# Optimization experiments

Hardware: AMD Instinct MI355X
Metric: run time of the kernel (lower is better)

Reference implementation:

```python
import jax, jax.numpy as jnp
import numpy as np

DIM = 1536; NH = 12; HD = 128; C2 = HD // 2          # rope half-dim = 64
F, H, W = 1, 30, 52
FRAME = H * W                                         # 1560 tokens/frame
SINK_FRAMES = 1; LOCAL_ATTN = 6
SINK = SINK_FRAMES * FRAME                            # 1560
MAX_ATTN = LOCAL_ATTN * 1560                          # 9360
CACHE = 9360                                          # kv cache length
GLOBAL_END = 9360; LOCAL_END_CACHE = 9360             # cache state before step
SPLITS = (C2 - 2 * (C2 // 3), C2 // 3, C2 // 3)       # (22, 21, 21)
EPS = 1e-6


def setup_inputs() -> dict:
    key = jax.random.key(0)
    ks = jax.random.split(key, 12)
    s = F * H * W
    rn = lambda k, sh, sc=1.0: jax.random.normal(k, sh, jnp.float32) * sc
    x = rn(ks[0], (1, s, DIM))
    Wq = rn(ks[1], (DIM, DIM), 0.02); Wk = rn(ks[2], (DIM, DIM), 0.02)
    Wv = rn(ks[3], (DIM, DIM), 0.02); Wo = rn(ks[4], (DIM, DIM), 0.02)
    zb = jnp.zeros((DIM,), jnp.float32)
    angles = jax.random.uniform(ks[5], (1024, C2), jnp.float32) * (2.0 * np.pi)
    freqs_cos = jnp.cos(angles); freqs_sin = jnp.sin(angles)
    cache_k = rn(ks[6], (1, CACHE, NH, HD)); cache_v = rn(ks[7], (1, CACHE, NH, HD))
    return dict(x=x, Wq=Wq, bq=zb, Wk=Wk, bk=zb, Wv=Wv, bv=zb, Wo=Wo, bo=zb,
                nq_w=jnp.ones((DIM,), jnp.float32), nk_w=jnp.ones((DIM,), jnp.float32),
                cache_k=cache_k, cache_v=cache_v,
                freqs_cos=freqs_cos, freqs_sin=freqs_sin,
                seq_lens=jnp.array([s], jnp.int32),
                grid_sizes=jnp.array([[F, H, W]], jnp.int32),
                current_start=GLOBAL_END)


def _rmsnorm(x, w):
    return x * jax.lax.rsqrt(jnp.mean(x * x, -1, keepdims=True) + EPS) * w


def _grid_table(table, start_frame):
    """table [1024, C2] -> per-token rope factors [S, 1, C2] over the (F,H,W) grid."""
    s0, s1, s2 = SPLITS
    tf, th, tw = table[:, :s0], table[:, s0:s0 + s1], table[:, s0 + s1:]
    fp = jnp.broadcast_to(tf[start_frame:start_frame + F][:, None, None, :], (F, H, W, s0))
    hp = jnp.broadcast_to(th[:H][None, :, None, :], (F, H, W, s1))
    wp = jnp.broadcast_to(tw[:W][None, None, :, :], (F, H, W, s2))
    return jnp.concatenate([fp, hp, wp], -1).reshape(F * H * W, 1, C2)


def _rope(x, cos, sin):
    # x: [b, s, n, d]; cos/sin: [s, 1, C2] (complex multiply in real arithmetic)
    b, s, n, d = x.shape
    xp = x.reshape(b, s, n, d // 2, 2)
    xr, xi = xp[..., 0], xp[..., 1]
    c, sn = cos[None], sin[None]                      # [1, s, 1, C2]
    out_r = xr * c - xi * sn
    out_i = xr * sn + xi * c
    return jnp.stack([out_r, out_i], -1).reshape(b, s, n, d)


def reference(x, Wq, bq, Wk, bk, Wv, bv, Wo, bo, nq_w, nk_w,
              cache_k, cache_v, freqs_cos, freqs_sin,
              seq_lens, grid_sizes, current_start):
    b, s = x.shape[:2]
    q = _rmsnorm(x @ Wq.T + bq, nq_w).reshape(b, s, NH, HD)
    k = _rmsnorm(x @ Wk.T + bk, nk_w).reshape(b, s, NH, HD)
    v = (x @ Wv.T + bv).reshape(b, s, NH, HD)

    start_frame = int(current_start) // FRAME
    cos = _grid_table(freqs_cos, start_frame)
    sin = _grid_table(freqs_sin, start_frame)
    rq = _rope(q, cos, sin)
    rk = _rope(k, cos, sin)

    # --- static cache bookkeeping (roll_and_insert path; all Python ints) ---
    num_new = s
    current_end = int(current_start) + num_new
    num_evicted = num_new + LOCAL_END_CACHE - CACHE           # 1560
    num_rolled = LOCAL_END_CACHE - num_evicted - SINK         # 6240
    local_end = LOCAL_END_CACHE + current_end - GLOBAL_END - num_evicted  # 9360
    local_start = local_end - num_new                         # 7800 == SINK + num_rolled
    temp_k = jnp.concatenate(
        [cache_k[:, :SINK], cache_k[:, SINK + num_evicted:SINK + num_evicted + num_rolled], rk], axis=1)
    temp_v = jnp.concatenate(
        [cache_v[:, :SINK], cache_v[:, SINK + num_evicted:SINK + num_evicted + num_rolled], v], axis=1)

    # --- sink + sliding-window attention ---
    local_budget = MAX_ATTN - SINK
    win_start = max(SINK, local_end - local_budget)
    k_cat = jnp.concatenate([temp_k[:, :SINK], temp_k[:, win_start:local_end]], axis=1)
    v_cat = jnp.concatenate([temp_v[:, :SINK], temp_v[:, win_start:local_end]], axis=1)

    logits = jnp.einsum('bqhd,bkhd->bhqk', rq, k_cat) * (HD ** -0.5)
    probs = jax.nn.softmax(logits, axis=-1)
    out = jnp.einsum('bhqk,bkhd->bqhd', probs, v_cat)
    y = out.reshape(b, s, DIM) @ Wo.T + bo
    return y
```

## Files before the change

### kernel.cpp

```cpp
#include <hip/hip_runtime.h>
#include <hip/hip_bf16.h>

typedef __bf16 bf16;
typedef __bf16 bf16x2 __attribute__((ext_vector_type(2)));
typedef __bf16 bf16x4 __attribute__((ext_vector_type(4)));
typedef __bf16 bf16x8 __attribute__((ext_vector_type(8)));
typedef float f32x4 __attribute__((ext_vector_type(4)));

#define DIM 1536
#define NH 12
#define HD 128
#define SEQ 1560
#define KV 9360
#define KVP 9408
#define SINK 1560
#define NEWBASE 7800
#define QSCALE 0.08838834764831845f
#define NSPLIT 3
#define CHUNK 3136
#define NT 49
#define QBLK 128
#define NQT 13

__device__ __forceinline__ void gl_lds16(const void* g, void* l) {
  __builtin_amdgcn_global_load_lds(
      (const __attribute__((address_space(1))) unsigned int*)g,
      (__attribute__((address_space(3))) unsigned int*)l, 16, 0, 0);
}

__global__ __launch_bounds__(256) void castk(const float* __restrict__ src,
                                             bf16* __restrict__ dst, int n) {
  int i = (blockIdx.x * 256 + threadIdx.x) * 8;
  if (i < n) {
    float4 a = *(const float4*)(src + i);
    float4 b = *(const float4*)(src + i + 4);
    bf16x8 o;
    o[0] = (bf16)a.x; o[1] = (bf16)a.y; o[2] = (bf16)a.z; o[3] = (bf16)a.w;
    o[4] = (bf16)b.x; o[5] = (bf16)b.y; o[6] = (bf16)b.z; o[7] = (bf16)b.w;
    *(bf16x8*)(dst + i) = o;
  }
}

struct GemmBatch {
  const bf16* B[3];
  const float* bias[3];
  float* C[3];
};

#define BM 128
#define BN 128
#define BK 32

__global__ __launch_bounds__(256, 2) void gemm_bt(const bf16* __restrict__ A,
                                                  GemmBatch gb, int M) {
  const bf16* Bw = gb.B[blockIdx.z];
  const float* bias = gb.bias[blockIdx.z];
  float* C = gb.C[blockIdx.z];
  int bm = blockIdx.x * BM;
  int bn = blockIdx.y * BN;

  __shared__ bf16 Alds[2][BM][BK];
  __shared__ bf16 Blds[2][BN][BK];

  int t = threadIdx.x;
  int lane = t & 63;
  int wave = t >> 6;
  int wr = wave >> 1, wc = wave & 1;
  int fr = lane & 15;
  int fo = (lane >> 4) * 8;

  f32x4 acc[4][4] = {};

  const int NK = DIM / BK;
  int colA = (lane & 3) * 8;
  int lrow = lane >> 2;

#define STAGEG(buf, k0)                                                     \
  {                                                                         \
    _Pragma("unroll") for (int p = 0; p < 2; ++p) {                         \
      int rbase = wave * 16 + p * 64;                                       \
      int ga = bm + rbase + lrow;                                           \
      if (ga > M - 1) ga = M - 1;                                           \
      gl_lds16(A + (size_t)ga * DIM + (k0) + colA, &Alds[buf][rbase][0]);   \
      int gbv = bn + rbase + lrow;                                          \
      gl_lds16(Bw + (size_t)gbv * DIM + (k0) + colA, &Blds[buf][rbase][0]); \
    }                                                                       \
  }

  STAGEG(0, 0);
  int cur = 0;
  for (int ks = 0; ks < NK; ++ks) {
    __syncthreads();
    if (ks + 1 < NK) STAGEG(cur ^ 1, (ks + 1) * BK);
    bf16x8 af[4], bfv[4];
#pragma unroll
    for (int i = 0; i < 4; ++i)
      af[i] = *(const bf16x8*)&Alds[cur][wr * 64 + i * 16 + fr][fo];
#pragma unroll
    for (int j = 0; j < 4; ++j)
      bfv[j] = *(const bf16x8*)&Blds[cur][wc * 64 + j * 16 + fr][fo];
#pragma unroll
    for (int i = 0; i < 4; ++i)
#pragma unroll
      for (int j = 0; j < 4; ++j)
        acc[i][j] = __builtin_amdgcn_mfma_f32_16x16x32_bf16(af[i], bfv[j],
                                                            acc[i][j], 0, 0, 0);
    cur ^= 1;
  }
#undef STAGEG

  int g4 = (lane >> 4) * 4;
#pragma unroll
  for (int i = 0; i < 4; ++i) {
    int mbase = bm + wr * 64 + i * 16 + g4;
#pragma unroll
    for (int j = 0; j < 4; ++j) {
      int col = bn + wc * 64 + j * 16 + fr;
      float bv = bias[col];
#pragma unroll
      for (int r = 0; r < 4; ++r) {
        int m = mbase + r;
        if (m < M) C[(size_t)m * DIM + col] = acc[i][j][r] + bv;
      }
    }
  }
}

__global__ __launch_bounds__(256) void norm_rope(
    const float* __restrict__ qraw, const float* __restrict__ kraw,
    const float* __restrict__ nqw, const float* __restrict__ nkw,
    const float* __restrict__ fcos, const float* __restrict__ fsin,
    bf16* __restrict__ Qh, bf16* __restrict__ Kcat) {
  int tok = blockIdx.x;
  int tid = threadIdx.x;
  const float* qr = qraw + (size_t)tok * DIM;
  const float* kr = kraw + (size_t)tok * DIM;
  float sq = 0.f, sk = 0.f;
  for (int c = tid; c < DIM; c += 256) {
    float a = qr[c];
    sq += a * a;
    float b = kr[c];
    sk += b * b;
  }
#pragma unroll
  for (int off = 32; off; off >>= 1) {
    sq += __shfl_down(sq, off);
    sk += __shfl_down(sk, off);
  }
  __shared__ float red[2][4];
  int w = tid >> 6;
  if ((tid & 63) == 0) {
    red[0][w] = sq;
    red[1][w] = sk;
  }
  __syncthreads();
  sq = red[0][0] + red[0][1] + red[0][2] + red[0][3];
  sk = red[1][0] + red[1][1] + red[1][2] + red[1][3];
  float rsq = rsqrtf(sq * (1.0f / DIM) + 1e-6f);
  float rsk = rsqrtf(sk * (1.0f / DIM) + 1e-6f);

  int hrow = tok / 52, wrow = tok % 52;
  for (int p = tid; p < NH * 64; p += 256) {
    int n = p >> 6, i = p & 63;
    int trow = (i < 22) ? 6 : (i < 43 ? hrow : wrow);
    float cs = fcos[trow * 64 + i];
    float sn = fsin[trow * 64 + i];
    int c = n * HD + 2 * i;
    float xr = qr[c] * rsq * nqw[c];
    float xi = qr[c + 1] * rsq * nqw[c + 1];
    bf16x2 qo;
    qo[0] = (bf16)((xr * cs - xi * sn) * QSCALE);
    qo[1] = (bf16)((xr * sn + xi * cs) * QSCALE);
    *(bf16x2*)(Qh + ((size_t)n * SEQ + tok) * HD + 2 * i) = qo;
    float yr = kr[c] * rsk * nkw[c];
    float yi = kr[c + 1] * rsk * nkw[c + 1];
    bf16x2 ko;
    ko[0] = (bf16)(yr * cs - yi * sn);
    ko[1] = (bf16)(yr * sn + yi * cs);
    *(bf16x2*)(Kcat + ((size_t)n * KVP + NEWBASE + tok) * HD + 2 * i) = ko;
  }
}

__global__ __launch_bounds__(256) void build_kcat(const float* __restrict__ cache_k,
                                                  bf16* __restrict__ Kcat) {
  int j = blockIdx.x;
  int src = j < SINK ? j : j + SINK;
  const float* sp = cache_k + (size_t)src * DIM;
  for (int c4 = threadIdx.x; c4 < DIM / 4; c4 += 256) {
    float4 v = *(const float4*)(sp + c4 * 4);
    int c = c4 * 4;
    int n = c >> 7, d = c & 127;
    bf16x4 o;
    o[0] = (bf16)v.x; o[1] = (bf16)v.y; o[2] = (bf16)v.z; o[3] = (bf16)v.w;
    *(bf16x4*)(Kcat + ((size_t)n * KVP + j) * HD + d) = o;
  }
}

__global__ __launch_bounds__(256) void build_vt(const float* __restrict__ cache_v,
                                                const float* __restrict__ vraw,
                                                bf16* __restrict__ Vt) {
  int h = blockIdx.y;
  int j0 = blockIdx.x * 64;
  __shared__ bf16 T[128][72];
  int tid = threadIdx.x;
  for (int idx = tid; idx < 64 * 32; idx += 256) {
    int jl = idx >> 5, s = idx & 31;
    int j = j0 + jl;
    if (j >= KV) continue;
    const float* sp;
    if (j < NEWBASE) {
      int srcj = j < SINK ? j : j + SINK;
      sp = cache_v + (size_t)srcj * DIM + h * HD;
    } else {
      sp = vraw + (size_t)(j - NEWBASE) * DIM + h * HD;
    }
    float4 v = *(const float4*)(sp + s * 4);
    T[s * 4 + 0][jl] = (bf16)v.x;
    T[s * 4 + 1][jl] = (bf16)v.y;
    T[s * 4 + 2][jl] = (bf16)v.z;
    T[s * 4 + 3][jl] = (bf16)v.w;
  }
  __syncthreads();
  for (int idx = tid; idx < 128 * 16; idx += 256) {
    int d = idx >> 4, g = idx & 15;
    int j = j0 + g * 4;
    if (j + 4 > KV) continue;
    bf16x4 o;
    o[0] = T[d][4 * g];
    o[1] = T[d][4 * g + 1];
    o[2] = T[d][4 * g + 2];
    o[3] = T[d][4 * g + 3];
    *(bf16x4*)(Vt + ((size_t)h * HD + d) * KVP + j) = o;
  }
}

__global__ __launch_bounds__(256, 2) void attn_split(const bf16* __restrict__ Qh,
                                                     const bf16* __restrict__ Kcat,
                                                     const bf16* __restrict__ Vt,
                                                     float* __restrict__ Opart,
                                                     float* __restrict__ MLpart) {
  int orig = blockIdx.x;
  int xcd = orig & 7, jj = orig >> 3;
  int wgid = (xcd < 4 ? xcd * 59 : 236 + (xcd - 4) * 58) + jj;
  int qt = wgid % NQT;
  int h = (wgid / NQT) % NH;
  int sp = wgid / (NQT * NH);
  int q0 = qt * QBLK;
  int c0 = sp * CHUNK;

  int t = threadIdx.x, lane = t & 63, w = t >> 6;
  int g = lane >> 4, fr = lane & 15, s3 = fr & 7;

  __shared__ bf16 Klds[2][64][128];
  __shared__ bf16 Vlds[2][128][64];
  __shared__ bf16 Plds[4][2][16][64];

  bf16x8 qf[2][4];
#pragma unroll
  for (int s = 0; s < 2; ++s) {
    int qrow = q0 + w * 32 + s * 16 + fr;
    int qcl = qrow < SEQ ? qrow : SEQ - 1;
    const bf16* Qp = Qh + ((size_t)h * SEQ + qcl) * HD + g * 8;
#pragma unroll
    for (int fk = 0; fk < 4; ++fk) qf[s][fk] = *(const bf16x8*)(Qp + 32 * fk);
  }

  int kadd[4], vadd[4];
#pragma unroll
  for (int p = 0; p < 4; ++p) {
    int m = (4 * w + p) * 64 + lane;
    int rK = m >> 4, cK = m & 15;
    kadd[p] = rK * HD + (cK ^ (rK & 7)) * 8;
    int dV = m >> 3, cV = m & 7;
    vadd[p] = dV * KVP + (cV ^ (dV & 7)) * 8;
  }
  char* Kbase = (char*)&Klds[0][0][0];
  char* Vbase = (char*)&Vlds[0][0][0];

  int koffr[4], voffc[2], poffc[2], pwb[4];
#pragma unroll
  for (int fk = 0; fk < 4; ++fk) koffr[fk] = fr * 256 + (((g + 4 * fk) ^ s3) * 16);
#pragma unroll
  for (int c = 0; c < 2; ++c) {
    voffc[c] = fr * 128 + (((g + 4 * c) ^ s3) * 16);
    poffc[c] = fr * 128 + (((4 * c + g) ^ s3) * 16);
  }
#pragma unroll
  for (int fj = 0; fj < 4; ++fj)
    pwb[fj] = fr * 128 + (((2 * fj + (g >> 1)) ^ s3) * 16) + (g & 1) * 8;
  char* PldsB0 = (char*)&Plds[w][0][0][0];
  char* PldsB1 = (char*)&Plds[w][1][0][0];

  const bf16* Khp = Kcat + (size_t)h * KVP * HD;
  const bf16* Vhp = Vt + (size_t)h * HD * KVP;

  f32x4 oacc[2][8] = {};
  float m_q[2] = {-1e30f, -1e30f};
  float l_q[2] = {0.f, 0.f};

#define STAGE(buf, j0)                                                   \
  {                                                                      \
    const bf16* Ks = Khp + (size_t)(j0)*HD;                              \
    const bf16* Vs = Vhp + (j0);                                         \
    _Pragma("unroll") for (int p = 0; p < 4; ++p)                        \
        gl_lds16(Ks + kadd[p], Kbase + (buf)*16384 + w * 4096 + p * 1024); \
    _Pragma("unroll") for (int p = 0; p < 4; ++p)                        \
        gl_lds16(Vs + vadd[p], Vbase + (buf)*16384 + w * 4096 + p * 1024); \
  }

  STAGE(0, c0);
  __syncthreads();
  int cur = 0;

  for (int ti = 0; ti < NT; ++ti) {
    int j0 = c0 + ti * 64;
    if (ti + 1 < NT) STAGE(cur ^ 1, j0 + 64);

    const char* Kc = Kbase + cur * 16384;
    const char* Vc = Vbase + cur * 16384;

    f32x4 sacc[2][4] = {};
    __builtin_amdgcn_s_setprio(1);
#pragma unroll
    for (int fj = 0; fj < 4; ++fj)
#pragma unroll
      for (int fk = 0; fk < 4; ++fk) {
        bf16x8 kf = *(const bf16x8*)(Kc + fj * 4096 + koffr[fk]);
        sacc[0][fj] = __builtin_amdgcn_mfma_f32_16x16x32_bf16(kf, qf[0][fk], sacc[0][fj], 0, 0, 0);
        sacc[1][fj] = __builtin_amdgcn_mfma_f32_16x16x32_bf16(kf, qf[1][fk], sacc[1][fj], 0, 0, 0);
      }
    __builtin_amdgcn_s_setprio(0);

    if (j0 + 64 > KV) {
#pragma unroll
      for (int fj = 0; fj < 4; ++fj)
#pragma unroll
        for (int r = 0; r < 4; ++r)
          if (j0 + 16 * fj + 4 * g + r >= KV) {
            sacc[0][fj][r] = -1e30f;
            sacc[1][fj][r] = -1e30f;
          }
    }

#pragma unroll
    for (int s = 0; s < 2; ++s) {
      float mx = sacc[s][0][0];
#pragma unroll
      for (int fj = 0; fj < 4; ++fj)
#pragma unroll
        for (int r = 0; r < 4; ++r)
          if (fj | r) mx = fmaxf(mx, sacc[s][fj][r]);
      mx = fmaxf(mx, __shfl_xor(mx, 16));
      mx = fmaxf(mx, __shfl_xor(mx, 32));
      float mnew = fmaxf(m_q[s], mx);
      float corr = __expf(m_q[s] - mnew);
      m_q[s] = mnew;
      float sum = 0.f;
      bf16x4 pw[4];
#pragma unroll
      for (int fj = 0; fj < 4; ++fj)
#pragma unroll
        for (int r = 0; r < 4; ++r) {
          float e = __expf(sacc[s][fj][r] - mnew);
          pw[fj][r] = (bf16)e;
          sum += e;
        }
      sum += __shfl_xor(sum, 16);
      sum += __shfl_xor(sum, 32);
      l_q[s] = l_q[s] * corr + sum;

      float corr_r[4];
#pragma unroll
      for (int r = 0; r < 4; ++r) corr_r[r] = __shfl(corr, 4 * g + r);
#pragma unroll
      for (int fd = 0; fd < 8; ++fd)
#pragma unroll
        for (int r = 0; r < 4; ++r) oacc[s][fd][r] *= corr_r[r];

      char* PB = s ? PldsB1 : PldsB0;
#pragma unroll
      for (int fj = 0; fj < 4; ++fj) *(bf16x4*)(PB + pwb[fj]) = pw[fj];
    }

    bf16x8 pa[2][2];
#pragma unroll
    for (int c = 0; c < 2; ++c) {
      pa[0][c] = *(const bf16x8*)(PldsB0 + poffc[c]);
      pa[1][c] = *(const bf16x8*)(PldsB1 + poffc[c]);
    }
    __builtin_amdgcn_s_setprio(1);
#pragma unroll
    for (int fd = 0; fd < 8; ++fd) {
      bf16x8 v0 = *(const bf16x8*)(Vc + fd * 2048 + voffc[0]);
      bf16x8 v1 = *(const bf16x8*)(Vc + fd * 2048 + voffc[1]);
      oacc[0][fd] = __builtin_amdgcn_mfma_f32_16x16x32_bf16(pa[0][0], v0, oacc[0][fd], 0, 0, 0);
      oacc[0][fd] = __builtin_amdgcn_mfma_f32_16x16x32_bf16(pa[0][1], v1, oacc[0][fd], 0, 0, 0);
      oacc[1][fd] = __builtin_amdgcn_mfma_f32_16x16x32_bf16(pa[1][0], v0, oacc[1][fd], 0, 0, 0);
      oacc[1][fd] = __builtin_amdgcn_mfma_f32_16x16x32_bf16(pa[1][1], v1, oacc[1][fd], 0, 0, 0);
    }
    __builtin_amdgcn_s_setprio(0);

    __syncthreads();
    cur ^= 1;
  }
#undef STAGE

  float* Oh = Opart + ((size_t)sp * NH + h) * SEQ * HD;
  float* MLh = MLpart + ((size_t)sp * NH + h) * SEQ * 2;
#pragma unroll
  for (int s = 0; s < 2; ++s) {
#pragma unroll
    for (int r = 0; r < 4; ++r) {
      int q = q0 + w * 32 + s * 16 + 4 * g + r;
      if (q >= SEQ) continue;
#pragma unroll
      for (int fd = 0; fd < 8; ++fd)
        Oh[(size_t)q * HD + fr + 16 * fd] = oacc[s][fd][r];
    }
  }
  if (lane < 16) {
#pragma unroll
    for (int s = 0; s < 2; ++s) {
      int q = q0 + w * 32 + s * 16 + lane;
      if (q < SEQ) {
        MLh[q * 2 + 0] = m_q[s];
        MLh[q * 2 + 1] = l_q[s];
      }
    }
  }
}

__global__ __launch_bounds__(256) void attn_merge(const float* __restrict__ Opart,
                                                  const float* __restrict__ MLpart,
                                                  bf16* __restrict__ Aout) {
  int idx = blockIdx.x * 2 + (threadIdx.x >> 7);
  if (idx >= NH * SEQ) return;
  int d = threadIdx.x & 127;
  int h = idx / SEQ, q = idx % SEQ;
  float m[NSPLIT];
  float M = -1e30f;
#pragma unroll
  for (int s = 0; s < NSPLIT; ++s) {
    m[s] = MLpart[(((size_t)s * NH + h) * SEQ + q) * 2];
    M = fmaxf(M, m[s]);
  }
  float L = 0.f, o = 0.f;
#pragma unroll
  for (int s = 0; s < NSPLIT; ++s) {
    float wgt = __expf(m[s] - M);
    L += MLpart[(((size_t)s * NH + h) * SEQ + q) * 2 + 1] * wgt;
    o += Opart[((((size_t)s * NH + h) * SEQ + q)) * HD + d] * wgt;
  }
  Aout[(size_t)q * DIM + h * HD + d] = (bf16)(o / L);
}

extern "C" void kernel_launch(void* const* d_in, const int* in_sizes, int n_in,
                              void* d_out, int out_size, void* d_ws, size_t ws_size,
                              hipStream_t stream) {
  const float* x = (const float*)d_in[0];
  const float* Wq = (const float*)d_in[1];
  const float* bq = (const float*)d_in[2];
  const float* Wk = (const float*)d_in[3];
  const float* bk = (const float*)d_in[4];
  const float* Wv = (const float*)d_in[5];
  const float* bv = (const float*)d_in[6];
  const float* Wo = (const float*)d_in[7];
  const float* bo = (const float*)d_in[8];
  const float* nqw = (const float*)d_in[9];
  const float* nkw = (const float*)d_in[10];
  const float* cache_k = (const float*)d_in[11];
  const float* cache_v = (const float*)d_in[12];
  const float* fcos = (const float*)d_in[13];
  const float* fsin = (const float*)d_in[14];
  float* out = (float*)d_out;

  char* ws = (char*)d_ws;
  size_t off = 0;
  auto alloc = [&](size_t bytes) {
    char* p = ws + off;
    off += (bytes + 255) & ~(size_t)255;
    return p;
  };
  const int XN = SEQ * DIM;
  const int WN = DIM * DIM;
  bf16* xb = (bf16*)alloc((size_t)XN * 2);
  bf16* Wqb = (bf16*)alloc((size_t)WN * 2);
  bf16* Wkb = (bf16*)alloc((size_t)WN * 2);
  bf16* Wvb = (bf16*)alloc((size_t)WN * 2);
  bf16* Wob = (bf16*)alloc((size_t)WN * 2);
  float* qraw = (float*)alloc((size_t)XN * 4);
  float* kraw = (float*)alloc((size_t)XN * 4);
  float* vraw = (float*)alloc((size_t)XN * 4);
  bf16* QhB = (bf16*)alloc((size_t)NH * SEQ * HD * 2);
  bf16* Kcat = (bf16*)alloc((size_t)NH * KVP * HD * 2);
  bf16* Vt = (bf16*)alloc((size_t)NH * HD * KVP * 2);
  bf16* Aout = (bf16*)alloc((size_t)XN * 2);
  float* Opart = (float*)alloc((size_t)NSPLIT * NH * SEQ * HD * 4);
  float* MLpart = (float*)alloc((size_t)NSPLIT * NH * SEQ * 2 * 4);

  castk<<<(XN + 2047) / 2048, 256, 0, stream>>>(x, xb, XN);
  castk<<<(WN + 2047) / 2048, 256, 0, stream>>>(Wq, Wqb, WN);
  castk<<<(WN + 2047) / 2048, 256, 0, stream>>>(Wk, Wkb, WN);
  castk<<<(WN + 2047) / 2048, 256, 0, stream>>>(Wv, Wvb, WN);
  castk<<<(WN + 2047) / 2048, 256, 0, stream>>>(Wo, Wob, WN);

  GemmBatch gqkv;
  gqkv.B[0] = Wqb; gqkv.B[1] = Wkb; gqkv.B[2] = Wvb;
  gqkv.bias[0] = bq; gqkv.bias[1] = bk; gqkv.bias[2] = bv;
  gqkv.C[0] = qraw; gqkv.C[1] = kraw; gqkv.C[2] = vraw;
  gemm_bt<<<dim3(13, 12, 3), 256, 0, stream>>>(xb, gqkv, SEQ);

  norm_rope<<<SEQ, 256, 0, stream>>>(qraw, kraw, nqw, nkw, fcos, fsin, QhB, Kcat);
  build_kcat<<<NEWBASE, 256, 0, stream>>>(cache_k, Kcat);
  build_vt<<<dim3(147, NH), 256, 0, stream>>>(cache_v, vraw, Vt);

  attn_split<<<dim3(NQT * NH * NSPLIT), 256, 0, stream>>>(QhB, Kcat, Vt, Opart, MLpart);
  attn_merge<<<(NH * SEQ + 1) / 2, 256, 0, stream>>>(Opart, MLpart, Aout);

  GemmBatch gout;
  gout.B[0] = Wob; gout.B[1] = Wob; gout.B[2] = Wob;
  gout.bias[0] = bo; gout.bias[1] = bo; gout.bias[2] = bo;
  gout.C[0] = out; gout.C[1] = out; gout.C[2] = out;
  gemm_bt<<<dim3(13, 12, 1), 256, 0, stream>>>(Aout, gout, SEQ);
}
```

Measured before the change: 305.9 us.

## Rework attention to 32x32 MFMA with register-resident P and lazy rescale

Rewrites the split attention kernel to use 32x32x16 bf16 MFMA tiles, so each wave handles 32 query rows with one accumulator set and builds the P operand through lane shuffles instead of an LDS round trip. The softmax switches to exp2 by folding log2(e) into the Q scale, and it skips the output rescale unless the running max rises by more than a threshold. The launch side merges the five cast kernels into one batched launch, aliases the q/k/v projection buffers onto the partial-output workspace, and adds a kernel that zeroes the K/V padding rows. The lazy rescale trades exactness of the running max for fewer multiplies, which risks overflow margins. The new swizzles and shuffles also add some complexity.

New measurement: 310.4 us. About the same (+1.5%).

```diff
diff --git a/kernel.cpp b/kernel.cpp
--- a/kernel.cpp
+++ b/kernel.cpp
@@ -6,6 +6,7 @@
 typedef __bf16 bf16x4 __attribute__((ext_vector_type(4)));
 typedef __bf16 bf16x8 __attribute__((ext_vector_type(8)));
 typedef float f32x4 __attribute__((ext_vector_type(4)));
+typedef float f32x16 __attribute__((ext_vector_type(16)));
 
 #define DIM 1536
 #define NH 12
@@ -15,7 +16,7 @@
 #define KVP 9408
 #define SINK 1560
 #define NEWBASE 7800
-#define QSCALE 0.08838834764831845f
+#define QSCALE_L2E (0.08838834764831845f * 1.4426950408889634f)
 #define NSPLIT 3
 #define CHUNK 3136
 #define NT 49
@@ -28,8 +29,19 @@
       (__attribute__((address_space(3))) unsigned int*)l, 16, 0, 0);
 }
 
-__global__ __launch_bounds__(256) void castk(const float* __restrict__ src,
-                                             bf16* __restrict__ dst, int n) {
+__device__ __forceinline__ f32x16 mfma32(bf16x8 a, bf16x8 b, f32x16 c) {
+  return __builtin_amdgcn_mfma_f32_32x32x16_bf16(a, b, c, 0, 0, 0);
+}
+
+struct CastBatch {
+  const float* src[5];
+  bf16* dst[5];
+  int n[5];
+};
+__global__ __launch_bounds__(256) void castall(CastBatch cb) {
+  const float* src = cb.src[blockIdx.y];
+  bf16* dst = cb.dst[blockIdx.y];
+  int n = cb.n[blockIdx.y];
   int i = (blockIdx.x * 256 + threadIdx.x) * 8;
   if (i < n) {
     float4 a = *(const float4*)(src + i);
@@ -38,6 +50,18 @@
     o[0] = (bf16)a.x; o[1] = (bf16)a.y; o[2] = (bf16)a.z; o[3] = (bf16)a.w;
     o[4] = (bf16)b.x; o[5] = (bf16)b.y; o[6] = (bf16)b.z; o[7] = (bf16)b.w;
     *(bf16x8*)(dst + i) = o;
+  }
+}
+
+__global__ __launch_bounds__(256) void clear_pad(bf16* __restrict__ Kcat,
+                                                 bf16* __restrict__ Vt) {
+  int h = blockIdx.y;
+  int i = blockIdx.x * 256 + threadIdx.x;
+  if (i < (KVP - KV) * HD) {
+    int r = KV + i / HD, d = i % HD;
+    Kcat[((size_t)h * KVP + r) * HD + d] = (bf16)0.f;
+    int dv = i / (KVP - KV), j = KV + i % (KVP - KV);
+    Vt[((size_t)h * HD + dv) * KVP + j] = (bf16)0.f;
   }
 }
 
@@ -169,8 +193,8 @@
     float xr = qr[c] * rsq * nqw[c];
     float xi = qr[c + 1] * rsq * nqw[c + 1];
     bf16x2 qo;
-    qo[0] = (bf16)((xr * cs - xi * sn) * QSCALE);
-    qo[1] = (bf16)((xr * sn + xi * cs) * QSCALE);
+    qo[0] = (bf16)((xr * cs - xi * sn) * QSCALE_L2E);
+    qo[1] = (bf16)((xr * sn + xi * cs) * QSCALE_L2E);
     *(bf16x2*)(Qh + ((size_t)n * SEQ + tok) * HD + 2 * i) = qo;
     float yr = kr[c] * rsk * nkw[c];
     float yi = kr[c + 1] * rsk * nkw[c + 1];
@@ -236,7 +260,7 @@
 
 __global__ __launch_bounds__(256, 2) void attn_split(const bf16* __restrict__ Qh,
                                                      const bf16* __restrict__ Kcat,
-                                                     const bf16* __restrict__ Vt,
+                                                     const bf16* __restrict__ Vtg,
                                                      float* __restrict__ Opart,
                                                      float* __restrict__ MLpart) {
   int orig = blockIdx.x;
@@ -249,63 +273,56 @@
   int c0 = sp * CHUNK;
 
   int t = threadIdx.x, lane = t & 63, w = t >> 6;
-  int g = lane >> 4, fr = lane & 15, s3 = fr & 7;
-
-  __shared__ bf16 Klds[2][64][128];
-  __shared__ bf16 Vlds[2][128][64];
-  __shared__ bf16 Plds[4][2][16][64];
-
-  bf16x8 qf[2][4];
-#pragma unroll
-  for (int s = 0; s < 2; ++s) {
-    int qrow = q0 + w * 32 + s * 16 + fr;
-    int qcl = qrow < SEQ ? qrow : SEQ - 1;
-    const bf16* Qp = Qh + ((size_t)h * SEQ + qcl) * HD + g * 8;
-#pragma unroll
-    for (int fk = 0; fk < 4; ++fk) qf[s][fk] = *(const bf16x8*)(Qp + 32 * fk);
-  }
+  int ql = lane & 31, hi = lane >> 5;
+
+  __shared__ __align__(16) bf16 Klds[2][64 * 128];
+  __shared__ __align__(16) bf16 Vlds[2][128 * 64];
+
+  int qrow = q0 + w * 32 + ql;
+  int qcl = qrow < SEQ ? qrow : SEQ - 1;
+  const bf16* Qp = Qh + ((size_t)h * SEQ + qcl) * HD + hi * 8;
+  bf16x8 qreg[8];
+#pragma unroll
+  for (int ks = 0; ks < 8; ++ks) qreg[ks] = *(const bf16x8*)(Qp + ks * 16);
 
   int kadd[4], vadd[4];
 #pragma unroll
   for (int p = 0; p < 4; ++p) {
-    int m = (4 * w + p) * 64 + lane;
-    int rK = m >> 4, cK = m & 15;
-    kadd[p] = rK * HD + (cK ^ (rK & 7)) * 8;
-    int dV = m >> 3, cV = m & 7;
-    vadd[p] = dV * KVP + (cV ^ (dV & 7)) * 8;
-  }
-  char* Kbase = (char*)&Klds[0][0][0];
-  char* Vbase = (char*)&Vlds[0][0][0];
-
-  int koffr[4], voffc[2], poffc[2], pwb[4];
-#pragma unroll
-  for (int fk = 0; fk < 4; ++fk) koffr[fk] = fr * 256 + (((g + 4 * fk) ^ s3) * 16);
-#pragma unroll
-  for (int c = 0; c < 2; ++c) {
-    voffc[c] = fr * 128 + (((g + 4 * c) ^ s3) * 16);
-    poffc[c] = fr * 128 + (((4 * c + g) ^ s3) * 16);
-  }
-#pragma unroll
-  for (int fj = 0; fj < 4; ++fj)
-    pwb[fj] = fr * 128 + (((2 * fj + (g >> 1)) ^ s3) * 16) + (g & 1) * 8;
-  char* PldsB0 = (char*)&Plds[w][0][0][0];
-  char* PldsB1 = (char*)&Plds[w][1][0][0];
+    int rK = (4 * w + p) * 4 + (lane >> 4);
+    int cK = (lane & 15) ^ (rK & 15);
+    kadd[p] = rK * HD + cK * 8;
+    int dV = (4 * w + p) * 8 + (lane >> 3);
+    int cV = (lane & 7) ^ (dV & 7);
+    vadd[p] = dV * KVP + cV * 8;
+  }
+
+  int koff[2][8];
+#pragma unroll
+  for (int kb = 0; kb < 2; ++kb)
+#pragma unroll
+    for (int ks = 0; ks < 8; ++ks)
+      koff[kb][ks] = (kb * 32 + ql) * 256 + (((ks * 2 + hi) ^ (ql & 15)) * 16);
+  int voff[4][4];
+#pragma unroll
+  for (int db = 0; db < 4; ++db)
+#pragma unroll
+    for (int ks = 0; ks < 4; ++ks)
+      voff[db][ks] = (db * 32 + ql) * 128 + (((ks * 2 + hi) ^ (ql & 7)) * 16);
 
   const bf16* Khp = Kcat + (size_t)h * KVP * HD;
-  const bf16* Vhp = Vt + (size_t)h * HD * KVP;
-
-  f32x4 oacc[2][8] = {};
-  float m_q[2] = {-1e30f, -1e30f};
-  float l_q[2] = {0.f, 0.f};
-
-#define STAGE(buf, j0)                                                   \
-  {                                                                      \
-    const bf16* Ks = Khp + (size_t)(j0)*HD;                              \
-    const bf16* Vs = Vhp + (j0);                                         \
-    _Pragma("unroll") for (int p = 0; p < 4; ++p)                        \
-        gl_lds16(Ks + kadd[p], Kbase + (buf)*16384 + w * 4096 + p * 1024); \
-    _Pragma("unroll") for (int p = 0; p < 4; ++p)                        \
-        gl_lds16(Vs + vadd[p], Vbase + (buf)*16384 + w * 4096 + p * 1024); \
+  const bf16* Vhp = Vtg + (size_t)h * HD * KVP;
+
+  f32x16 oacc[4] = {};
+  float m_q = -1e38f, l_q = 0.f;
+
+#define STAGE(buf, j0)                                                        \
+  {                                                                           \
+    const bf16* Ks = Khp + (size_t)(j0)*HD;                                   \
+    const bf16* Vs = Vhp + (j0);                                              \
+    _Pragma("unroll") for (int p = 0; p < 4; ++p) {                           \
+      gl_lds16(Ks + kadd[p], (char*)&Klds[buf][0] + w * 4096 + p * 1024);     \
+      gl_lds16(Vs + vadd[p], (char*)&Vlds[buf][0] + w * 4096 + p * 1024);     \
+    }                                                                         \
   }
 
   STAGE(0, c0);
@@ -316,88 +333,99 @@
     int j0 = c0 + ti * 64;
     if (ti + 1 < NT) STAGE(cur ^ 1, j0 + 64);
 
-    const char* Kc = Kbase + cur * 16384;
-    const char* Vc = Vbase + cur * 16384;
-
-    f32x4 sacc[2][4] = {};
+    const char* Kc = (const char*)&Klds[cur][0];
+    const char* Vc = (const char*)&Vlds[cur][0];
+
+    f32x16 s0 = {}, s1 = {};
     __builtin_amdgcn_s_setprio(1);
 #pragma unroll
-    for (int fj = 0; fj < 4; ++fj)
-#pragma unroll
-      for (int fk = 0; fk < 4; ++fk) {
-        bf16x8 kf = *(const bf16x8*)(Kc + fj * 4096 + koffr[fk]);
-        sacc[0][fj] = __builtin_amdgcn_mfma_f32_16x16x32_bf16(kf, qf[0][fk], sacc[0][fj], 0, 0, 0);
-        sacc[1][fj] = __builtin_amdgcn_mfma_f32_16x16x32_bf16(kf, qf[1][fk], sacc[1][fj], 0, 0, 0);
+    for (int ks = 0; ks < 8; ++ks) {
+      s0 = mfma32(*(const bf16x8*)(Kc + koff[0][ks]), qreg[ks], s0);
+      s1 = mfma32(*(const bf16x8*)(Kc + koff[1][ks]), qreg[ks], s1);
+    }
+    __builtin_amdgcn_s_setprio(0);
+
+    if (j0 + 64 > KV) {
+#pragma unroll
+      for (int reg = 0; reg < 16; ++reg) {
+        int kk = (reg & 3) + 8 * (reg >> 2) + 4 * hi;
+        if (j0 + kk >= KV) s0[reg] = -1e38f;
+        if (j0 + 32 + kk >= KV) s1[reg] = -1e38f;
       }
-    __builtin_amdgcn_s_setprio(0);
-
-    if (j0 + 64 > KV) {
-#pragma unroll
-      for (int fj = 0; fj < 4; ++fj)
-#pragma unroll
-        for (int r = 0; r < 4; ++r)
-          if (j0 + 16 * fj + 4 * g + r >= KV) {
-            sacc[0][fj][r] = -1e30f;
-            sacc[1][fj][r] = -1e30f;
-          }
-    }
-
-#pragma unroll
-    for (int s = 0; s < 2; ++s) {
-      float mx = sacc[s][0][0];
-#pragma unroll
-      for (int fj = 0; fj < 4; ++fj)
-#pragma unroll
-        for (int r = 0; r < 4; ++r)
-          if (fj | r) mx = fmaxf(mx, sacc[s][fj][r]);
-      mx = fmaxf(mx, __shfl_xor(mx, 16));
-      mx = fmaxf(mx, __shfl_xor(mx, 32));
-      float mnew = fmaxf(m_q[s], mx);
-      float corr = __expf(m_q[s] - mnew);
-      m_q[s] = mnew;
-      float sum = 0.f;
-      bf16x4 pw[4];
-#pragma unroll
-      for (int fj = 0; fj < 4; ++fj)
-#pragma unroll
-        for (int r = 0; r < 4; ++r) {
-          float e = __expf(sacc[s][fj][r] - mnew);
-          pw[fj][r] = (bf16)e;
-          sum += e;
-        }
-      sum += __shfl_xor(sum, 16);
-      sum += __shfl_xor(sum, 32);
-      l_q[s] = l_q[s] * corr + sum;
-
-      float corr_r[4];
-#pragma unroll
-      for (int r = 0; r < 4; ++r) corr_r[r] = __shfl(corr, 4 * g + r);
-#pragma unroll
-      for (int fd = 0; fd < 8; ++fd)
-#pragma unroll
-        for (int r = 0; r < 4; ++r) oacc[s][fd][r] *= corr_r[r];
-
-      char* PB = s ? PldsB1 : PldsB0;
-#pragma unroll
-      for (int fj = 0; fj < 4; ++fj) *(bf16x4*)(PB + pwb[fj]) = pw[fj];
-    }
-
-    bf16x8 pa[2][2];
-#pragma unroll
-    for (int c = 0; c < 2; ++c) {
-      pa[0][c] = *(const bf16x8*)(PldsB0 + poffc[c]);
-      pa[1][c] = *(const bf16x8*)(PldsB1 + poffc[c]);
-    }
+    }
+
+    f32x16 mm;
+#pragma unroll
+    for (int r = 0; r < 16; ++r) mm[r] = fmaxf(s0[r], s1[r]);
+    float m8[8];
+#pragma unroll
+    for (int r = 0; r < 8; ++r) m8[r] = fmaxf(mm[r], mm[r + 8]);
+    float mx = fmaxf(fmaxf(fmaxf(m8[0], m8[4]), fmaxf(m8[1], m8[5])),
+                     fmaxf(fmaxf(m8[2], m8[6]), fmaxf(m8[3], m8[7])));
+    mx = fmaxf(mx, __shfl_xor(mx, 32));
+
+    if (__any(mx - m_q > 8.f)) {
+      float mnew = fmaxf(m_q, mx);
+      float corr = exp2f(m_q - mnew);
+      m_q = mnew;
+      l_q *= corr;
+#pragma unroll
+      for (int reg = 0; reg < 16; ++reg) {
+        int qsrc = (reg & 3) + 8 * (reg >> 2) + 4 * hi;
+        float c = __shfl(corr, qsrc);
+#pragma unroll
+        for (int db = 0; db < 4; ++db) oacc[db][reg] *= c;
+      }
+    }
+
+#pragma unroll
+    for (int r = 0; r < 16; ++r) {
+      s0[r] = exp2f(s0[r] - m_q);
+      s1[r] = exp2f(s1[r] - m_q);
+    }
+    f32x16 ss;
+#pragma unroll
+    for (int r = 0; r < 16; ++r) ss[r] = s0[r] + s1[r];
+    float t8[8];
+#pragma unroll
+    for (int r = 0; r < 8; ++r) t8[r] = ss[r] + ss[r + 8];
+    float sum = ((t8[0] + t8[4]) + (t8[1] + t8[5])) +
+                ((t8[2] + t8[6]) + (t8[3] + t8[7]));
+    sum += __shfl_xor(sum, 32);
+    l_q += sum;
+
+    bf16x8 pa[4];
+#pragma unroll
+    for (int ks = 0; ks < 4; ++ks) {
+      const f32x16& S = (ks < 2) ? s0 : s1;
+      const int r0 = (ks & 1) * 8;
+      bf16x2 p0, p1, p2, p3;
+      p0[0] = (bf16)S[r0 + 0]; p0[1] = (bf16)S[r0 + 1];
+      p1[0] = (bf16)S[r0 + 2]; p1[1] = (bf16)S[r0 + 3];
+      p2[0] = (bf16)S[r0 + 4]; p2[1] = (bf16)S[r0 + 5];
+      p3[0] = (bf16)S[r0 + 6]; p3[1] = (bf16)S[r0 + 7];
+      int x0 = __builtin_bit_cast(int, p0);
+      int x1 = __builtin_bit_cast(int, p1);
+      int y0 = __builtin_bit_cast(int, p2);
+      int y1 = __builtin_bit_cast(int, p3);
+      int sx0 = __shfl_xor(x0, 32);
+      int sx1 = __shfl_xor(x1, 32);
+      int sy0 = __shfl_xor(y0, 32);
+      int sy1 = __shfl_xor(y1, 32);
+      int4 tmp;
+      tmp.x = hi ? sy0 : x0;
+      tmp.y = hi ? sy1 : x1;
+      tmp.z = hi ? y0 : sx0;
+      tmp.w = hi ? y1 : sx1;
+      pa[ks] = __builtin_bit_cast(bf16x8, tmp);
+    }
+
     __builtin_amdgcn_s_setprio(1);
 #pragma unroll
-    for (int fd = 0; fd < 8; ++fd) {
-      bf16x8 v0 = *(const bf16x8*)(Vc + fd * 2048 + voffc[0]);
-      bf16x8 v1 = *(const bf16x8*)(Vc + fd * 2048 + voffc[1]);
-      oacc[0][fd] = __builtin_amdgcn_mfma_f32_16x16x32_bf16(pa[0][0], v0, oacc[0][fd], 0, 0, 0);
-      oacc[0][fd] = __builtin_amdgcn_mfma_f32_16x16x32_bf16(pa[0][1], v1, oacc[0][fd], 0, 0, 0);
-      oacc[1][fd] = __builtin_amdgcn_mfma_f32_16x16x32_bf16(pa[1][0], v0, oacc[1][fd], 0, 0, 0);
-      oacc[1][fd] = __builtin_amdgcn_mfma_f32_16x16x32_bf16(pa[1][1], v1, oacc[1][fd], 0, 0, 0);
-    }
+    for (int db = 0; db < 4; ++db)
+#pragma unroll
+      for (int ks = 0; ks < 4; ++ks)
+        oacc[db] = mfma32(pa[ks], *(const bf16x8*)(Vc + voff[db][ks]), oacc[db]);
     __builtin_amdgcn_s_setprio(0);
 
     __syncthreads();
@@ -408,24 +436,18 @@
   float* Oh = Opart + ((size_t)sp * NH + h) * SEQ * HD;
   float* MLh = MLpart + ((size_t)sp * NH + h) * SEQ * 2;
 #pragma unroll
-  for (int s = 0; s < 2; ++s) {
-#pragma unroll
-    for (int r = 0; r < 4; ++r) {
-      int q = q0 + w * 32 + s * 16 + 4 * g + r;
-      if (q >= SEQ) continue;
-#pragma unroll
-      for (int fd = 0; fd < 8; ++fd)
-        Oh[(size_t)q * HD + fr + 16 * fd] = oacc[s][fd][r];
-    }
-  }
-  if (lane < 16) {
-#pragma unroll
-    for (int s = 0; s < 2; ++s) {
-      int q = q0 + w * 32 + s * 16 + lane;
-      if (q < SEQ) {
-        MLh[q * 2 + 0] = m_q[s];
-        MLh[q * 2 + 1] = l_q[s];
-      }
+  for (int reg = 0; reg < 16; ++reg) {
+    int q = q0 + w * 32 + (reg & 3) + 8 * (reg >> 2) + 4 * hi;
+    if (q >= SEQ) continue;
+#pragma unroll
+    for (int db = 0; db < 4; ++db)
+      Oh[(size_t)q * HD + db * 32 + ql] = oacc[db][reg];
+  }
+  if (lane < 32) {
+    int q = q0 + w * 32 + ql;
+    if (q < SEQ) {
+      MLh[q * 2 + 0] = m_q;
+      MLh[q * 2 + 1] = l_q;
     }
   }
 }
@@ -438,7 +460,7 @@
   int d = threadIdx.x & 127;
   int h = idx / SEQ, q = idx % SEQ;
   float m[NSPLIT];
-  float M = -1e30f;
+  float M = -1e38f;
 #pragma unroll
   for (int s = 0; s < NSPLIT; ++s) {
     m[s] = MLpart[(((size_t)s * NH + h) * SEQ + q) * 2];
@@ -447,7 +469,7 @@
   float L = 0.f, o = 0.f;
 #pragma unroll
   for (int s = 0; s < NSPLIT; ++s) {
-    float wgt = __expf(m[s] - M);
+    float wgt = exp2f(m[s] - M);
     L += MLpart[(((size_t)s * NH + h) * SEQ + q) * 2 + 1] * wgt;
     o += Opart[((((size_t)s * NH + h) * SEQ + q)) * HD + d] * wgt;
   }
@@ -488,21 +510,25 @@
   bf16* Wkb = (bf16*)alloc((size_t)WN * 2);
   bf16* Wvb = (bf16*)alloc((size_t)WN * 2);
   bf16* Wob = (bf16*)alloc((size_t)WN * 2);
-  float* qraw = (float*)alloc((size_t)XN * 4);
-  float* kraw = (float*)alloc((size_t)XN * 4);
-  float* vraw = (float*)alloc((size_t)XN * 4);
   bf16* QhB = (bf16*)alloc((size_t)NH * SEQ * HD * 2);
   bf16* Kcat = (bf16*)alloc((size_t)NH * KVP * HD * 2);
   bf16* Vt = (bf16*)alloc((size_t)NH * HD * KVP * 2);
   bf16* Aout = (bf16*)alloc((size_t)XN * 2);
+  float* MLpart = (float*)alloc((size_t)NSPLIT * NH * SEQ * 2 * 4);
   float* Opart = (float*)alloc((size_t)NSPLIT * NH * SEQ * HD * 4);
-  float* MLpart = (float*)alloc((size_t)NSPLIT * NH * SEQ * 2 * 4);
-
-  castk<<<(XN + 2047) / 2048, 256, 0, stream>>>(x, xb, XN);
-  castk<<<(WN + 2047) / 2048, 256, 0, stream>>>(Wq, Wqb, WN);
-  castk<<<(WN + 2047) / 2048, 256, 0, stream>>>(Wk, Wkb, WN);
-  castk<<<(WN + 2047) / 2048, 256, 0, stream>>>(Wv, Wvb, WN);
-  castk<<<(WN + 2047) / 2048, 256, 0, stream>>>(Wo, Wob, WN);
+  float* qraw = Opart;
+  float* kraw = qraw + XN;
+  float* vraw = kraw + XN;
+
+  CastBatch cb;
+  cb.src[0] = x;  cb.dst[0] = xb;  cb.n[0] = XN;
+  cb.src[1] = Wq; cb.dst[1] = Wqb; cb.n[1] = WN;
+  cb.src[2] = Wk; cb.dst[2] = Wkb; cb.n[2] = WN;
+  cb.src[3] = Wv; cb.dst[3] = Wvb; cb.n[3] = WN;
+  cb.src[4] = Wo; cb.dst[4] = Wob; cb.n[4] = WN;
+  castall<<<dim3((XN + 2047) / 2048, 5), 256, 0, stream>>>(cb);
+
+  clear_pad<<<dim3(((KVP - KV) * HD + 255) / 256, NH), 256, 0, stream>>>(Kcat, Vt);
 
   GemmBatch gqkv;
   gqkv.B[0] = Wqb; gqkv.B[1] = Wkb; gqkv.B[2] = Wvb;
```
